# Performance work log

Measured on AMD Instinct MI355X. Metric: run time of the kernel, lower is better.

The kernel has to match this reference:

```python
import jax, jax.numpy as jnp
import numpy as np

D_MODEL = 512
NUM_HEADS = 8
D_K = D_MODEL // NUM_HEADS
SCALE = 1.0 / np.sqrt(D_K).astype(np.float32)


def _relative_shift(x):
    # x: (B, H, S, P) pos scores from Q @ P^T; Transformer-XL shift trick.
    b, h, s, p = x.shape
    x = jnp.pad(x, ((0, 0), (0, 0), (0, 0), (1, 0)))   # (B,H,S,P+1)
    x = x.reshape(b, h, p + 1, s)[:, :, 1:, :]          # drop first row
    x = x.reshape(b, h, s, p)[:, :, :, :s]
    return x


def setup_inputs() -> dict:
    key = jax.random.key(0)
    ks = jax.random.split(key, 10)
    B, S = 4, 2048
    glorot = lambda k: jax.random.uniform(
        k, (D_MODEL, D_MODEL), jnp.float32,
        -np.sqrt(6.0 / (2 * D_MODEL)), np.sqrt(6.0 / (2 * D_MODEL)))
    return {
        "inputs": jax.random.normal(ks[0], (B, S, D_MODEL), jnp.float32),
        "pos_enc": jax.random.normal(ks[1], (1, S, D_MODEL), jnp.float32),
        "W_q": glorot(ks[2]),
        "W_k": glorot(ks[3]),
        "W_v": glorot(ks[4]),
        "W_o": glorot(ks[5]),
        "W_pos": glorot(ks[6]),
        "u_bias": jnp.zeros((NUM_HEADS, D_K), jnp.float32),
        "v_bias": jnp.zeros((NUM_HEADS, D_K), jnp.float32),
    }


def reference(inputs, pos_enc, W_q, W_k, W_v, W_o, W_pos, u_bias, v_bias):
    B, S, _ = inputs.shape
    split = lambda x, b: x.reshape(b, S, NUM_HEADS, D_K).transpose(0, 2, 1, 3)
    Q = split(inputs @ W_q, B)        # (B,H,S,dk)
    K = split(inputs @ W_k, B)
    V = split(inputs @ W_v, B)
    P = split(pos_enc @ W_pos, 1)      # (1,H,S,dk)
    u = u_bias[None, :, None, :]
    v = v_bias[None, :, None, :]
    content_score = jnp.einsum('bhid,bhjd->bhij', Q + u, K)
    pos_score = jnp.einsum('bhid,xhjd->bhij', Q + v, P)  # broadcast over batch
    pos_score = _relative_shift(pos_score)
    scores = (content_score + pos_score) * SCALE
    attn = jax.nn.softmax(scores, axis=-1)  # no dropout (inference)
    context = jnp.einsum('bhij,bhjd->bhid', attn, V)
    context = context.transpose(0, 2, 1, 3).reshape(B, S, D_MODEL)
    return context @ W_o
```

## Files before the change

kernel.cpp:

```cpp
#include <hip/hip_runtime.h>
#include <hip/hip_bf16.h>
#include <math.h>

#define SEQ 2048
#define NH 8
#define DK 64
#define DM 512
#define RSCALE 0.125f
#define PPAD (SEQ + 128)
#define POFF 64
#define KSTR 72
#define PSTR 36

typedef unsigned short ushortT;
typedef short s16x8 __attribute__((ext_vector_type(8)));
typedef float f32x4 __attribute__((ext_vector_type(4)));

#define MFMA16 __builtin_amdgcn_mfma_f32_16x16x32_bf16

static __device__ __forceinline__ ushortT f2bf(float x) {
  __hip_bfloat16 h = __float2bfloat16(x);
  ushortT u;
  __builtin_memcpy(&u, &h, 2);
  return u;
}

static __device__ __forceinline__ f32x4 exp4(f32x4 g) {
  f32x4 r;
  r[0] = __expf(g[0]); r[1] = __expf(g[1]);
  r[2] = __expf(g[2]); r[3] = __expf(g[3]);
  return r;
}

static __device__ __forceinline__ s16x8 pack8(const float* p) {
  ushortT u[8];
#pragma unroll
  for (int i = 0; i < 8; ++i) u[i] = f2bf(p[i]);
  s16x8 out;
  __builtin_memcpy(&out, u, 16);
  return out;
}

static __device__ __forceinline__ int pinv(int j) {
  return (j < 16) ? ((j >> 2) * 8 + (j & 3)) : (((j >> 2) - 4) * 8 + 4 + (j & 3));
}

__global__ __launch_bounds__(256)
void cast_in(const float* __restrict__ X, const float* __restrict__ PE,
             ushortT* __restrict__ Xb, ushortT* __restrict__ PEb) {
  const size_t i4 = (size_t)blockIdx.x * 256 + threadIdx.x;
  const size_t NX = (size_t)4 * SEQ * DM / 4;
  const float4 v = (i4 < NX) ? *(const float4*)(X + i4 * 4)
                             : *(const float4*)(PE + (i4 - NX) * 4);
  ushortT o[4] = {f2bf(v.x), f2bf(v.y), f2bf(v.z), f2bf(v.w)};
  ushortT* dst = (i4 < NX) ? (Xb + i4 * 4) : (PEb + (i4 - NX) * 4);
  *(ulonglong1*)dst = *(ulonglong1*)o;
}

__global__ __launch_bounds__(256)
void transpose_w(const float* __restrict__ w0, const float* __restrict__ w1,
                 const float* __restrict__ w2, const float* __restrict__ w3,
                 const float* __restrict__ w4, ushortT* __restrict__ out) {
  __shared__ float ts[32][33];
  const int z = blockIdx.z;
  const float* w = (z == 0) ? w0 : (z == 1) ? w1 : (z == 2) ? w2 : (z == 3) ? w3 : w4;
  ushortT* o = out + (size_t)z * DM * DM;
  const int k0 = blockIdx.x * 32, n0 = blockIdx.y * 32;
  const int tx = threadIdx.x, ty = threadIdx.y;
#pragma unroll
  for (int i = 0; i < 4; ++i)
    ts[ty + i * 8][tx] = w[(size_t)(k0 + ty + i * 8) * DM + n0 + tx];
  __syncthreads();
#pragma unroll
  for (int i = 0; i < 4; ++i)
    o[(size_t)(n0 + ty + i * 8) * DM + k0 + tx] = f2bf(ts[tx][ty + i * 8]);
}

__global__ __launch_bounds__(256)
void gemm_mfma(const ushortT* __restrict__ A, const ushortT* __restrict__ Bt,
               const float* __restrict__ ubv, const float* __restrict__ vbv,
               ushortT* __restrict__ qu, ushortT* __restrict__ qv,
               ushortT* __restrict__ kb, ushortT* __restrict__ vt,
               float* __restrict__ of, int mode) {
  const int w = threadIdx.x >> 6, lane = threadIdx.x & 63;
  const int c = lane & 15, q = lane >> 4;
  const int m0 = blockIdx.x * 64;
  const int n0 = blockIdx.y * 128 + w * 32;

  const ushortT* Ab = A + (size_t)m0 * DM + q * 8;
  const ushortT* Bb = Bt + (size_t)n0 * DM + q * 8;

  f32x4 acc[4][2];
#pragma unroll
  for (int mt = 0; mt < 4; ++mt)
#pragma unroll
    for (int nt = 0; nt < 2; ++nt) acc[mt][nt] = (f32x4){0.f, 0.f, 0.f, 0.f};

  s16x8 a[4], bfr[2], an[4], bn[2];
#pragma unroll
  for (int mt = 0; mt < 4; ++mt) a[mt] = *(const s16x8*)(Ab + (size_t)(mt * 16 + c) * DM);
#pragma unroll
  for (int nt = 0; nt < 2; ++nt) bfr[nt] = *(const s16x8*)(Bb + (size_t)(nt * 16 + c) * DM);

  for (int k0 = 0; k0 < DM; k0 += 32) {
    if (k0 + 32 < DM) {
#pragma unroll
      for (int mt = 0; mt < 4; ++mt)
        an[mt] = *(const s16x8*)(Ab + (size_t)(mt * 16 + c) * DM + k0 + 32);
#pragma unroll
      for (int nt = 0; nt < 2; ++nt)
        bn[nt] = *(const s16x8*)(Bb + (size_t)(nt * 16 + c) * DM + k0 + 32);
    }
#pragma unroll
    for (int mt = 0; mt < 4; ++mt)
#pragma unroll
      for (int nt = 0; nt < 2; ++nt)
        acc[mt][nt] = MFMA16(a[mt], bfr[nt], acc[mt][nt], 0, 0, 0);
#pragma unroll
    for (int mt = 0; mt < 4; ++mt) a[mt] = an[mt];
#pragma unroll
    for (int nt = 0; nt < 2; ++nt) bfr[nt] = bn[nt];
  }

#pragma unroll
  for (int mt = 0; mt < 4; ++mt)
#pragma unroll
    for (int nt = 0; nt < 2; ++nt)
#pragma unroll
      for (int r = 0; r < 4; ++r) {
        const int gm = m0 + mt * 16 + q * 4 + r;
        const int gn = n0 + nt * 16 + c;
        const float v = acc[mt][nt][r];
        const int bb = gm >> 11, s = gm & (SEQ - 1);
        if (mode == 0) {
          const int z = gn >> 9, gn5 = gn & 511;
          const int h = gn5 >> 6, d = gn5 & 63;
          if (z == 0) {
            const size_t base = (((size_t)bb * NH + h) * SEQ + s) * DK + d;
            qu[base] = f2bf((v + ubv[gn5]) * RSCALE);
            qv[base] = f2bf((v + vbv[gn5]) * RSCALE);
          } else if (z == 1) {
            kb[(((size_t)bb * NH + h) * SEQ + s) * DK + d] = f2bf(v);
          } else {
            const int s_il = (s & ~31) | pinv(s & 31);
            vt[(((size_t)bb * NH + h) * DK + d) * SEQ + s_il] = f2bf(v);
          }
        } else if (mode == 3) {
          const int h = gn >> 6, d = gn & 63;
          qu[((size_t)h * PPAD + POFF + gm) * DK + d] = f2bf(v);
        } else {
          of[(size_t)gm * DM + gn] = v;
        }
      }
}

static __device__ __forceinline__ f32x4 band_gemm(const ushortT* pb, int tile,
                                                  int c, int q, s16x8 a0, s16x8 a1) {
  const ushortT* pc = pb + (ptrdiff_t)(tile * 16 + c) * DK + q * 8;
  f32x4 G = {0.f, 0.f, 0.f, 0.f};
  G = MFMA16(a0, *(const s16x8*)pc, G, 0, 0, 0);
  G = MFMA16(a1, *(const s16x8*)(pc + 32), G, 0, 0, 0);
  return G;
}

__global__ __launch_bounds__(256, 3)
void attn_mfma(const ushortT* __restrict__ Qu, const ushortT* __restrict__ Qv,
               const ushortT* __restrict__ Kb, const ushortT* __restrict__ Vt,
               const ushortT* __restrict__ Pp, ushortT* __restrict__ ctxb) {
  const int n = blockIdx.x;
  const int xcd = n & 7, idx = n >> 3;
  const int b = idx >> 5, iblk = idx & 31;
  const int h = xcd, bh = b * 8 + h;
  const int tid = threadIdx.x;
  const int w = tid >> 6, lane = tid & 63;
  const int c = lane & 15, q = lane >> 4;
  const int i0 = iblk * 64;
  const int iw = i0 + w * 16;

  __shared__ ushortT Ks[64][KSTR];
  __shared__ ushortT Vs[64][KSTR];
  __shared__ float E1[4][16][PSTR];
  __shared__ float E2[4][16][PSTR];
  __shared__ float Lb[4][16];

  const ushortT* Qub = Qu + ((size_t)bh * SEQ + iw) * DK;
  const ushortT* Qvb = Qv + ((size_t)bh * SEQ + iw) * DK;
  const ushortT* Kbh = Kb + (size_t)bh * SEQ * DK;
  const ushortT* Vbh = Vt + (size_t)bh * DK * SEQ;
  const ushortT* Ph  = Pp + ((size_t)h * PPAD + POFF) * DK;

  const s16x8 qu0 = *(const s16x8*)(Qub + (size_t)c * DK + q * 8);
  const s16x8 qu1 = *(const s16x8*)(Qub + (size_t)c * DK + 32 + q * 8);
  s16x8 qv0 = *(const s16x8*)(Qvb + (size_t)c * DK + q * 8);
  s16x8 qv1 = *(const s16x8*)(Qvb + (size_t)c * DK + 32 + q * 8);

  int joff[8];
#pragma unroll
  for (int jj = 0; jj < 8; ++jj)
    joff[jj] = (jj < 4) ? (4 * q + jj) : (16 + 4 * q + (jj - 4));

  f32x4 O[4];
#pragma unroll
  for (int r = 0; r < 4; ++r) O[r] = (f32x4){0.f, 0.f, 0.f, 0.f};
  float lrow = 0.f;
  f32x4 e[3];
  bool hv1 = false, hv2 = false;
  const int jt = iw & ~31;
  const int m_w = q * 4;

  {
    const ushortT* gk = Kbh;
    uint4 k0v = *(const uint4*)(gk + tid * 8);
    uint4 k1v = *(const uint4*)(gk + 2048 + tid * 8);
    const ushortT* gv = Vbh + (size_t)(tid >> 2) * SEQ + (tid & 3) * 16;
    uint4 v0v = *(const uint4*)gv;
    uint4 v1v = *(const uint4*)(gv + 8);
    *(uint4*)&Ks[tid >> 3][(tid & 7) * 8] = k0v;
    *(uint4*)&Ks[32 + (tid >> 3)][(tid & 7) * 8] = k1v;
    *(uint4*)&Vs[tid >> 2][(tid & 3) * 16] = v0v;
    *(uint4*)&Vs[tid >> 2][(tid & 3) * 16 + 8] = v1v;
  }
  __syncthreads();

#define WRITE_BAND(ARR, ev)                                                   \
  _Pragma("unroll")                                                           \
  for (int t = 0; t < 3; ++t)                                                 \
    _Pragma("unroll")                                                         \
    for (int r = 0; r < 4; ++r) {                                             \
      const int kcol = t * 16 + c + (m_w + r) - 15;                           \
      if (kcol >= 0 && kcol < 32) ARR[w][m_w + r][pinv(kcol)] = (ev)[t][r];   \
    }

#define PV_FROM(pr, jl)                                                       \
  {                                                                           \
    lrow += pr[0] + pr[1] + pr[2] + pr[3] + pr[4] + pr[5] + pr[6] + pr[7];    \
    const s16x8 pa = pack8(pr);                                               \
    _Pragma("unroll")                                                         \
    for (int dt = 0; dt < 4; ++dt) {                                          \
      const s16x8 vb = *(const s16x8*)&Vs[dt * 16 + c][(jl) + q * 8];         \
      O[dt] = MFMA16(pa, vb, O[dt], 0, 0, 0);                                 \
    }                                                                         \
  }

  for (int ch = 0; ch < 32; ++ch) {
    const bool more = (ch + 1) < 32;
    uint4 k0v, k1v, v0v, v1v;
    if (more) {
      const ushortT* gk = Kbh + (size_t)(ch + 1) * 64 * DK;
      k0v = *(const uint4*)(gk + tid * 8);
      k1v = *(const uint4*)(gk + 2048 + tid * 8);
      const ushortT* gv = Vbh + (size_t)(tid >> 2) * SEQ + (ch + 1) * 64 + (tid & 3) * 16;
      v0v = *(const uint4*)gv;
      v1v = *(const uint4*)(gv + 8);
    }
#pragma unroll
    for (int t = 0; t < 2; ++t) {
      const int j0 = ch * 64 + t * 32;
      const int jl = t * 32;
      const int drel = j0 - iw;
      f32x4 S0 = {0.f, 0.f, 0.f, 0.f}, S1 = {0.f, 0.f, 0.f, 0.f};
      {
        const ushortT* ka = &Ks[jl + c][q * 8];
        S0 = MFMA16(*(const s16x8*)ka, qu0, S0, 0, 0, 0);
        S0 = MFMA16(*(const s16x8*)(ka + 32), qu1, S0, 0, 0, 0);
        const ushortT* ka2 = &Ks[jl + 16 + c][q * 8];
        S1 = MFMA16(*(const s16x8*)ka2, qu0, S1, 0, 0, 0);
        S1 = MFMA16(*(const s16x8*)(ka2 + 32), qu1, S1, 0, 0, 0);
      }
      if (j0 < jt) {
        const ushortT* pb1 = Ph + (ptrdiff_t)(drel + SEQ - 16) * DK;
        if (hv1) e[0] = e[2];
        else { e[0] = exp4(band_gemm(pb1, 0, c, q, qv0, qv1)); hv1 = true; }
        e[1] = exp4(band_gemm(pb1, 1, c, q, qv0, qv1));
        e[2] = exp4(band_gemm(pb1, 2, c, q, qv0, qv1));
        WRITE_BAND(E1, e)
        const float* e1r = &E1[w][c][q * 8];
        float4 fA = *(const float4*)e1r, fB = *(const float4*)(e1r + 4);
        float pr[8] = {__expf(S0[0]) * fA.x, __expf(S0[1]) * fA.y,
                       __expf(S0[2]) * fA.z, __expf(S0[3]) * fA.w,
                       __expf(S1[0]) * fB.x, __expf(S1[1]) * fB.y,
                       __expf(S1[2]) * fB.z, __expf(S1[3]) * fB.w};
        PV_FROM(pr, jl)
      } else if (j0 < jt + 64) {
        {
          const ushortT* pb1 = Ph + (ptrdiff_t)(drel + SEQ - 16) * DK;
          f32x4 t1[3];
          t1[0] = exp4(band_gemm(pb1, 0, c, q, qv0, qv1));
          t1[1] = exp4(band_gemm(pb1, 1, c, q, qv0, qv1));
          t1[2] = exp4(band_gemm(pb1, 2, c, q, qv0, qv1));
          WRITE_BAND(E1, t1)
        }
        {
          const s16x8 qw0 = *(const s16x8*)(Qvb + (size_t)(c + 1) * DK + q * 8);
          const s16x8 qw1 = *(const s16x8*)(Qvb + (size_t)(c + 1) * DK + 32 + q * 8);
          const ushortT* pb2 = Ph + (ptrdiff_t)(drel - 17) * DK;
          f32x4 t2[3];
          t2[0] = exp4(band_gemm(pb2, 0, c, q, qw0, qw1));
          t2[1] = exp4(band_gemm(pb2, 1, c, q, qw0, qw1));
          t2[2] = exp4(band_gemm(pb2, 2, c, q, qw0, qw1));
          WRITE_BAND(E2, t2)
        }
        const float* e1r = &E1[w][c][q * 8];
        const float* e2r = &E2[w][c][q * 8];
        float4 aA = *(const float4*)e1r, aB = *(const float4*)(e1r + 4);
        float4 bA = *(const float4*)e2r, bB = *(const float4*)(e2r + 4);
        float f1[8] = {aA.x, aA.y, aA.z, aA.w, aB.x, aB.y, aB.z, aB.w};
        float f2[8] = {bA.x, bA.y, bA.z, bA.w, bB.x, bB.y, bB.z, bB.w};
        float es[8] = {__expf(S0[0]), __expf(S0[1]), __expf(S0[2]), __expf(S0[3]),
                       __expf(S1[0]), __expf(S1[1]), __expf(S1[2]), __expf(S1[3])};
        float pr[8];
#pragma unroll
        for (int jj = 0; jj < 8; ++jj) {
          const int dlt = drel + joff[jj] - c;
          const float f = (dlt <= 0) ? f1[jj] : ((dlt == 1) ? 1.0f : f2[jj]);
          pr[jj] = es[jj] * f;
        }
        PV_FROM(pr, jl)
      } else {
        if (!hv2) {
          qv0 = *(const s16x8*)(Qvb + (size_t)(c + 1) * DK + q * 8);
          qv1 = *(const s16x8*)(Qvb + (size_t)(c + 1) * DK + 32 + q * 8);
        }
        const ushortT* pb2 = Ph + (ptrdiff_t)(drel - 17) * DK;
        if (hv2) e[0] = e[2];
        else { e[0] = exp4(band_gemm(pb2, 0, c, q, qv0, qv1)); hv2 = true; }
        e[1] = exp4(band_gemm(pb2, 1, c, q, qv0, qv1));
        e[2] = exp4(band_gemm(pb2, 2, c, q, qv0, qv1));
        WRITE_BAND(E1, e)
        const float* e1r = &E1[w][c][q * 8];
        float4 fA = *(const float4*)e1r, fB = *(const float4*)(e1r + 4);
        float pr[8] = {__expf(S0[0]) * fA.x, __expf(S0[1]) * fA.y,
                       __expf(S0[2]) * fA.z, __expf(S0[3]) * fA.w,
                       __expf(S1[0]) * fB.x, __expf(S1[1]) * fB.y,
                       __expf(S1[2]) * fB.z, __expf(S1[3]) * fB.w};
        PV_FROM(pr, jl)
      }
    }
    __syncthreads();
    if (more) {
      *(uint4*)&Ks[tid >> 3][(tid & 7) * 8] = k0v;
      *(uint4*)&Ks[32 + (tid >> 3)][(tid & 7) * 8] = k1v;
      *(uint4*)&Vs[tid >> 2][(tid & 3) * 16] = v0v;
      *(uint4*)&Vs[tid >> 2][(tid & 3) * 16 + 8] = v1v;
    }
    __syncthreads();
  }

  lrow += __shfl_xor(lrow, 16);
  lrow += __shfl_xor(lrow, 32);
  if (q == 0) Lb[w][c] = lrow;
  float inv[4];
#pragma unroll
  for (int r = 0; r < 4; ++r) inv[r] = 1.0f / Lb[w][q * 4 + r];
#pragma unroll
  for (int dt = 0; dt < 4; ++dt)
#pragma unroll
    for (int r = 0; r < 4; ++r) {
      const int i = iw + q * 4 + r;
      ctxb[((size_t)b * SEQ + i) * DM + h * DK + dt * 16 + c] = f2bf(O[dt][r] * inv[r]);
    }
}

extern "C" void kernel_launch(void* const* d_in, const int* in_sizes, int n_in,
                              void* d_out, int out_size, void* d_ws, size_t ws_size,
                              hipStream_t stream) {
  (void)in_sizes; (void)n_in; (void)out_size; (void)ws_size;
  const float* X   = (const float*)d_in[0];
  const float* PE  = (const float*)d_in[1];
  const float* Wq  = (const float*)d_in[2];
  const float* Wk  = (const float*)d_in[3];
  const float* Wv  = (const float*)d_in[4];
  const float* Wo  = (const float*)d_in[5];
  const float* Wp  = (const float*)d_in[6];
  const float* ubv = (const float*)d_in[7];
  const float* vbv = (const float*)d_in[8];

  const size_t NX = (size_t)4 * SEQ * DM;
  const size_t NP = (size_t)SEQ * DM;
  const size_t NW = (size_t)DM * DM;
  ushortT* Xb  = (ushortT*)d_ws;
  ushortT* PEb = Xb + NX;
  ushortT* Wt  = PEb + NP;
  ushortT* qu  = Wt + 5 * NW;
  ushortT* qv  = qu + NX;
  ushortT* kb  = qv + NX;
  ushortT* vt  = kb + NX;
  ushortT* pp  = vt + NX;
  ushortT* ctx = pp + (size_t)NH * PPAD * DK;
  float* outp = (float*)d_out;

  hipLaunchKernelGGL(cast_in, dim3((NX + NP) / 4 / 256), dim3(256), 0, stream, X, PE, Xb, PEb);
  hipLaunchKernelGGL(transpose_w, dim3(16, 16, 5), dim3(32, 8), 0, stream, Wq, Wk, Wv, Wp, Wo, Wt);
  dim3 blk(256);
  hipLaunchKernelGGL(gemm_mfma, dim3(128, 12), blk, 0, stream, Xb, Wt, ubv, vbv,
                     qu, qv, kb, vt, (float*)nullptr, 0);
  hipLaunchKernelGGL(gemm_mfma, dim3(32, 4), blk, 0, stream, PEb, Wt + 3 * NW, ubv, vbv,
                     pp, (ushortT*)nullptr, (ushortT*)nullptr, (ushortT*)nullptr, (float*)nullptr, 3);
  hipLaunchKernelGGL(attn_mfma, dim3(1024), blk, 0, stream, qu, qv, kb, vt, pp, ctx);
  hipLaunchKernelGGL(gemm_mfma, dim3(128, 4), blk, 0, stream, ctx, Wt + 4 * NW, ubv, vbv,
                     (ushortT*)nullptr, (ushortT*)nullptr, (ushortT*)nullptr, (ushortT*)nullptr, outp, 4);
}
```

Baseline: 408.1 us.

## Double-buffer K in LDS, read V from global, drop E2 buffer for occupancy

V tiles are no longer staged in shared memory; PV MFMA operands are loaded directly from global/L2. K is double-buffered in LDS, which removes one barrier per chunk, and the second band scratch buffer is replaced by reusing E1 sequentially. Launch bounds rise from 3 to 5 blocks per SM to exploit the smaller LDS footprint. The cost is uncoalesced per-lane global V loads and higher register pressure from the tighter launch bound.

```diff
diff --git a/kernel.cpp b/kernel.cpp
--- a/kernel.cpp
+++ b/kernel.cpp
@@ -163,7 +163,7 @@
   return G;
 }
 
-__global__ __launch_bounds__(256, 3)
+__global__ __launch_bounds__(256, 5)
 void attn_mfma(const ushortT* __restrict__ Qu, const ushortT* __restrict__ Qv,
                const ushortT* __restrict__ Kb, const ushortT* __restrict__ Vt,
                const ushortT* __restrict__ Pp, ushortT* __restrict__ ctxb) {
@@ -177,10 +177,8 @@
   const int i0 = iblk * 64;
   const int iw = i0 + w * 16;
 
-  __shared__ ushortT Ks[64][KSTR];
-  __shared__ ushortT Vs[64][KSTR];
+  __shared__ ushortT Ks[2][64][KSTR];
   __shared__ float E1[4][16][PSTR];
-  __shared__ float E2[4][16][PSTR];
   __shared__ float Lb[4][16];
 
   const ushortT* Qub = Qu + ((size_t)bh * SEQ + iw) * DK;
@@ -209,49 +207,41 @@
   const int m_w = q * 4;
 
   {
-    const ushortT* gk = Kbh;
-    uint4 k0v = *(const uint4*)(gk + tid * 8);
-    uint4 k1v = *(const uint4*)(gk + 2048 + tid * 8);
-    const ushortT* gv = Vbh + (size_t)(tid >> 2) * SEQ + (tid & 3) * 16;
-    uint4 v0v = *(const uint4*)gv;
-    uint4 v1v = *(const uint4*)(gv + 8);
-    *(uint4*)&Ks[tid >> 3][(tid & 7) * 8] = k0v;
-    *(uint4*)&Ks[32 + (tid >> 3)][(tid & 7) * 8] = k1v;
-    *(uint4*)&Vs[tid >> 2][(tid & 3) * 16] = v0v;
-    *(uint4*)&Vs[tid >> 2][(tid & 3) * 16 + 8] = v1v;
+    uint4 k0v = *(const uint4*)(Kbh + tid * 8);
+    uint4 k1v = *(const uint4*)(Kbh + 2048 + tid * 8);
+    *(uint4*)&Ks[0][tid >> 3][(tid & 7) * 8] = k0v;
+    *(uint4*)&Ks[0][32 + (tid >> 3)][(tid & 7) * 8] = k1v;
   }
   __syncthreads();
 
-#define WRITE_BAND(ARR, ev)                                                   \
+#define WRITE_BAND(ev)                                                        \
   _Pragma("unroll")                                                           \
   for (int t = 0; t < 3; ++t)                                                 \
     _Pragma("unroll")                                                         \
     for (int r = 0; r < 4; ++r) {                                             \
       const int kcol = t * 16 + c + (m_w + r) - 15;                           \
-      if (kcol >= 0 && kcol < 32) ARR[w][m_w + r][pinv(kcol)] = (ev)[t][r];   \
-    }
-
-#define PV_FROM(pr, jl)                                                       \
+      if (kcol >= 0 && kcol < 32) E1[w][m_w + r][pinv(kcol)] = (ev)[t][r];    \
+    }
+
+#define PV_FROM(pr, j0g)                                                      \
   {                                                                           \
     lrow += pr[0] + pr[1] + pr[2] + pr[3] + pr[4] + pr[5] + pr[6] + pr[7];    \
     const s16x8 pa = pack8(pr);                                               \
     _Pragma("unroll")                                                         \
     for (int dt = 0; dt < 4; ++dt) {                                          \
-      const s16x8 vb = *(const s16x8*)&Vs[dt * 16 + c][(jl) + q * 8];         \
+      const s16x8 vb = *(const s16x8*)(Vbh + (size_t)(dt * 16 + c) * SEQ + (j0g) + q * 8); \
       O[dt] = MFMA16(pa, vb, O[dt], 0, 0, 0);                                 \
     }                                                                         \
   }
 
   for (int ch = 0; ch < 32; ++ch) {
+    const int cur = ch & 1;
     const bool more = (ch + 1) < 32;
-    uint4 k0v, k1v, v0v, v1v;
+    uint4 k0v, k1v;
     if (more) {
       const ushortT* gk = Kbh + (size_t)(ch + 1) * 64 * DK;
       k0v = *(const uint4*)(gk + tid * 8);
       k1v = *(const uint4*)(gk + 2048 + tid * 8);
-      const ushortT* gv = Vbh + (size_t)(tid >> 2) * SEQ + (ch + 1) * 64 + (tid & 3) * 16;
-      v0v = *(const uint4*)gv;
-      v1v = *(const uint4*)(gv + 8);
     }
 #pragma unroll
     for (int t = 0; t < 2; ++t) {
@@ -260,10 +250,10 @@
       const int drel = j0 - iw;
       f32x4 S0 = {0.f, 0.f, 0.f, 0.f}, S1 = {0.f, 0.f, 0.f, 0.f};
       {
-        const ushortT* ka = &Ks[jl + c][q * 8];
+        const ushortT* ka = &Ks[cur][jl + c][q * 8];
         S0 = MFMA16(*(const s16x8*)ka, qu0, S0, 0, 0, 0);
         S0 = MFMA16(*(const s16x8*)(ka + 32), qu1, S0, 0, 0, 0);
-        const ushortT* ka2 = &Ks[jl + 16 + c][q * 8];
+        const ushortT* ka2 = &Ks[cur][jl + 16 + c][q * 8];
         S1 = MFMA16(*(const s16x8*)ka2, qu0, S1, 0, 0, 0);
         S1 = MFMA16(*(const s16x8*)(ka2 + 32), qu1, S1, 0, 0, 0);
       }
@@ -273,22 +263,27 @@
         else { e[0] = exp4(band_gemm(pb1, 0, c, q, qv0, qv1)); hv1 = true; }
         e[1] = exp4(band_gemm(pb1, 1, c, q, qv0, qv1));
         e[2] = exp4(band_gemm(pb1, 2, c, q, qv0, qv1));
-        WRITE_BAND(E1, e)
+        WRITE_BAND(e)
         const float* e1r = &E1[w][c][q * 8];
         float4 fA = *(const float4*)e1r, fB = *(const float4*)(e1r + 4);
         float pr[8] = {__expf(S0[0]) * fA.x, __expf(S0[1]) * fA.y,
                        __expf(S0[2]) * fA.z, __expf(S0[3]) * fA.w,
                        __expf(S1[0]) * fB.x, __expf(S1[1]) * fB.y,
                        __expf(S1[2]) * fB.z, __expf(S1[3]) * fB.w};
-        PV_FROM(pr, jl)
+        PV_FROM(pr, j0)
       } else if (j0 < jt + 64) {
+        float f1[8], f2[8];
         {
           const ushortT* pb1 = Ph + (ptrdiff_t)(drel + SEQ - 16) * DK;
           f32x4 t1[3];
           t1[0] = exp4(band_gemm(pb1, 0, c, q, qv0, qv1));
           t1[1] = exp4(band_gemm(pb1, 1, c, q, qv0, qv1));
           t1[2] = exp4(band_gemm(pb1, 2, c, q, qv0, qv1));
-          WRITE_BAND(E1, t1)
+          WRITE_BAND(t1)
+          const float* e1r = &E1[w][c][q * 8];
+          float4 aA = *(const float4*)e1r, aB = *(const float4*)(e1r + 4);
+          f1[0] = aA.x; f1[1] = aA.y; f1[2] = aA.z; f1[3] = aA.w;
+          f1[4] = aB.x; f1[5] = aB.y; f1[6] = aB.z; f1[7] = aB.w;
         }
         {
           const s16x8 qw0 = *(const s16x8*)(Qvb + (size_t)(c + 1) * DK + q * 8);
@@ -298,14 +293,12 @@
           t2[0] = exp4(band_gemm(pb2, 0, c, q, qw0, qw1));
           t2[1] = exp4(band_gemm(pb2, 1, c, q, qw0, qw1));
           t2[2] = exp4(band_gemm(pb2, 2, c, q, qw0, qw1));
-          WRITE_BAND(E2, t2)
-        }
-        const float* e1r = &E1[w][c][q * 8];
-        const float* e2r = &E2[w][c][q * 8];
-        float4 aA = *(const float4*)e1r, aB = *(const float4*)(e1r + 4);
-        float4 bA = *(const float4*)e2r, bB = *(const float4*)(e2r + 4);
-        float f1[8] = {aA.x, aA.y, aA.z, aA.w, aB.x, aB.y, aB.z, aB.w};
-        float f2[8] = {bA.x, bA.y, bA.z, bA.w, bB.x, bB.y, bB.z, bB.w};
+          WRITE_BAND(t2)
+          const float* e1r = &E1[w][c][q * 8];
+          float4 bA = *(const float4*)e1r, bB = *(const float4*)(e1r + 4);
+          f2[0] = bA.x; f2[1] = bA.y; f2[2] = bA.z; f2[3] = bA.w;
+          f2[4] = bB.x; f2[5] = bB.y; f2[6] = bB.z; f2[7] = bB.w;
+        }
         float es[8] = {__expf(S0[0]), __expf(S0[1]), __expf(S0[2]), __expf(S0[3]),
                        __expf(S1[0]), __expf(S1[1]), __expf(S1[2]), __expf(S1[3])};
         float pr[8];
@@ -315,7 +308,7 @@
           const float f = (dlt <= 0) ? f1[jj] : ((dlt == 1) ? 1.0f : f2[jj]);
           pr[jj] = es[jj] * f;
         }
-        PV_FROM(pr, jl)
+        PV_FROM(pr, j0)
       } else {
         if (!hv2) {
           qv0 = *(const s16x8*)(Qvb + (size_t)(c + 1) * DK + q * 8);
@@ -326,22 +319,19 @@
         else { e[0] = exp4(band_gemm(pb2, 0, c, q, qv0, qv1)); hv2 = true; }
         e[1] = exp4(band_gemm(pb2, 1, c, q, qv0, qv1));
         e[2] = exp4(band_gemm(pb2, 2, c, q, qv0, qv1));
-        WRITE_BAND(E1, e)
+        WRITE_BAND(e)
         const float* e1r = &E1[w][c][q * 8];
         float4 fA = *(const float4*)e1r, fB = *(const float4*)(e1r + 4);
         float pr[8] = {__expf(S0[0]) * fA.x, __expf(S0[1]) * fA.y,
                        __expf(S0[2]) * fA.z, __expf(S0[3]) * fA.w,
                        __expf(S1[0]) * fB.x, __expf(S1[1]) * fB.y,
                        __expf(S1[2]) * fB.z, __expf(S1[3]) * fB.w};
-        PV_FROM(pr, jl)
+        PV_FROM(pr, j0)
       }
     }
-    __syncthreads();
     if (more) {
-      *(uint4*)&Ks[tid >> 3][(tid & 7) * 8] = k0v;
-      *(uint4*)&Ks[32 + (tid >> 3)][(tid & 7) * 8] = k1v;
-      *(uint4*)&Vs[tid >> 2][(tid & 3) * 16] = v0v;
-      *(uint4*)&Vs[tid >> 2][(tid & 3) * 16 + 8] = v1v;
+      *(uint4*)&Ks[1 - cur][tid >> 3][(tid & 7) * 8] = k0v;
+      *(uint4*)&Ks[1 - cur][32 + (tid >> 3)][(tid & 7) * 8] = k1v;
     }
     __syncthreads();
   }
```

After: 640.3 us. +56.9%, slower.

## Stage GEMM operands through LDS with 128x128 block tiles

Applied to the files above, without the earlier changes.

Rewrites the projection GEMM so each 256-thread block loads a 128x128 output tile's A and B k-slices cooperatively into padded shared memory, then each wave reads its MFMA fragments from LDS. Before, each wave loaded its fragments straight from global memory with no sharing across waves. The change is meant to cut redundant global/L2 traffic by reusing operands across the four waves, and it doubles the per-wave tile to 64x64. The cost is two barriers per k-step, fewer blocks in the grid (lower occupancy on the small pos GEMM), and more accumulator registers.

```diff
diff --git a/kernel.cpp b/kernel.cpp
--- a/kernel.cpp
+++ b/kernel.cpp
@@ -11,6 +11,7 @@
 #define POFF 64
 #define KSTR 72
 #define PSTR 36
+#define ASTR 34
 
 typedef unsigned short ushortT;
 typedef short s16x8 __attribute__((ext_vector_type(8)));
@@ -82,54 +83,61 @@
                ushortT* __restrict__ qu, ushortT* __restrict__ qv,
                ushortT* __restrict__ kb, ushortT* __restrict__ vt,
                float* __restrict__ of, int mode) {
-  const int w = threadIdx.x >> 6, lane = threadIdx.x & 63;
+  __shared__ ushortT As[128][ASTR];
+  __shared__ ushortT Bs[128][ASTR];
+  const int tid = threadIdx.x;
+  const int w = tid >> 6, lane = tid & 63;
   const int c = lane & 15, q = lane >> 4;
-  const int m0 = blockIdx.x * 64;
-  const int n0 = blockIdx.y * 128 + w * 32;
-
-  const ushortT* Ab = A + (size_t)m0 * DM + q * 8;
-  const ushortT* Bb = Bt + (size_t)n0 * DM + q * 8;
-
-  f32x4 acc[4][2];
+  const int wm = w >> 1, wn = w & 1;
+  const int m0 = blockIdx.x * 128, n0 = blockIdx.y * 128;
+  const int lr = tid >> 1, lh = (tid & 1) * 16;
+
+  f32x4 acc[4][4];
 #pragma unroll
   for (int mt = 0; mt < 4; ++mt)
 #pragma unroll
-    for (int nt = 0; nt < 2; ++nt) acc[mt][nt] = (f32x4){0.f, 0.f, 0.f, 0.f};
-
-  s16x8 a[4], bfr[2], an[4], bn[2];
-#pragma unroll
-  for (int mt = 0; mt < 4; ++mt) a[mt] = *(const s16x8*)(Ab + (size_t)(mt * 16 + c) * DM);
-#pragma unroll
-  for (int nt = 0; nt < 2; ++nt) bfr[nt] = *(const s16x8*)(Bb + (size_t)(nt * 16 + c) * DM);
+    for (int nt = 0; nt < 4; ++nt) acc[mt][nt] = (f32x4){0.f, 0.f, 0.f, 0.f};
+
+  const ushortT* Ar = A + (size_t)(m0 + lr) * DM + lh;
+  const ushortT* Br = Bt + (size_t)(n0 + lr) * DM + lh;
+  uint4 a0 = *(const uint4*)(Ar);
+  uint4 a1 = *(const uint4*)(Ar + 8);
+  uint4 b0 = *(const uint4*)(Br);
+  uint4 b1 = *(const uint4*)(Br + 8);
 
   for (int k0 = 0; k0 < DM; k0 += 32) {
+    __syncthreads();
+    *(uint4*)&As[lr][lh] = a0; *(uint4*)&As[lr][lh + 8] = a1;
+    *(uint4*)&Bs[lr][lh] = b0; *(uint4*)&Bs[lr][lh + 8] = b1;
+    __syncthreads();
     if (k0 + 32 < DM) {
-#pragma unroll
-      for (int mt = 0; mt < 4; ++mt)
-        an[mt] = *(const s16x8*)(Ab + (size_t)(mt * 16 + c) * DM + k0 + 32);
-#pragma unroll
-      for (int nt = 0; nt < 2; ++nt)
-        bn[nt] = *(const s16x8*)(Bb + (size_t)(nt * 16 + c) * DM + k0 + 32);
-    }
+      a0 = *(const uint4*)(Ar + k0 + 32);
+      a1 = *(const uint4*)(Ar + k0 + 40);
+      b0 = *(const uint4*)(Br + k0 + 32);
+      b1 = *(const uint4*)(Br + k0 + 40);
+    }
+    s16x8 af[4], bf[4];
 #pragma unroll
     for (int mt = 0; mt < 4; ++mt)
-#pragma unroll
-      for (int nt = 0; nt < 2; ++nt)
-        acc[mt][nt] = MFMA16(a[mt], bfr[nt], acc[mt][nt], 0, 0, 0);
-#pragma unroll
-    for (int mt = 0; mt < 4; ++mt) a[mt] = an[mt];
-#pragma unroll
-    for (int nt = 0; nt < 2; ++nt) bfr[nt] = bn[nt];
+      af[mt] = *(const s16x8*)&As[wm * 64 + mt * 16 + c][q * 8];
+#pragma unroll
+    for (int nt = 0; nt < 4; ++nt)
+      bf[nt] = *(const s16x8*)&Bs[wn * 64 + nt * 16 + c][q * 8];
+#pragma unroll
+    for (int mt = 0; mt < 4; ++mt)
+#pragma unroll
+      for (int nt = 0; nt < 4; ++nt)
+        acc[mt][nt] = MFMA16(af[mt], bf[nt], acc[mt][nt], 0, 0, 0);
   }
 
 #pragma unroll
   for (int mt = 0; mt < 4; ++mt)
 #pragma unroll
-    for (int nt = 0; nt < 2; ++nt)
+    for (int nt = 0; nt < 4; ++nt)
 #pragma unroll
       for (int r = 0; r < 4; ++r) {
-        const int gm = m0 + mt * 16 + q * 4 + r;
-        const int gn = n0 + nt * 16 + c;
+        const int gm = m0 + wm * 64 + mt * 16 + q * 4 + r;
+        const int gn = n0 + wn * 64 + nt * 16 + c;
         const float v = acc[mt][nt][r];
         const int bb = gm >> 11, s = gm & (SEQ - 1);
         if (mode == 0) {
@@ -392,11 +400,11 @@
   hipLaunchKernelGGL(cast_in, dim3((NX + NP) / 4 / 256), dim3(256), 0, stream, X, PE, Xb, PEb);
   hipLaunchKernelGGL(transpose_w, dim3(16, 16, 5), dim3(32, 8), 0, stream, Wq, Wk, Wv, Wp, Wo, Wt);
   dim3 blk(256);
-  hipLaunchKernelGGL(gemm_mfma, dim3(128, 12), blk, 0, stream, Xb, Wt, ubv, vbv,
+  hipLaunchKernelGGL(gemm_mfma, dim3(64, 12), blk, 0, stream, Xb, Wt, ubv, vbv,
                      qu, qv, kb, vt, (float*)nullptr, 0);
-  hipLaunchKernelGGL(gemm_mfma, dim3(32, 4), blk, 0, stream, PEb, Wt + 3 * NW, ubv, vbv,
+  hipLaunchKernelGGL(gemm_mfma, dim3(16, 4), blk, 0, stream, PEb, Wt + 3 * NW, ubv, vbv,
                      pp, (ushortT*)nullptr, (ushortT*)nullptr, (ushortT*)nullptr, (float*)nullptr, 3);
   hipLaunchKernelGGL(attn_mfma, dim3(1024), blk, 0, stream, qu, qv, kb, vt, pp, ctx);
-  hipLaunchKernelGGL(gemm_mfma, dim3(128, 4), blk, 0, stream, ctx, Wt + 4 * NW, ubv, vbv,
+  hipLaunchKernelGGL(gemm_mfma, dim3(64, 4), blk, 0, stream, ctx, Wt + 4 * NW, ubv, vbv,
                      (ushortT*)nullptr, (ushortT*)nullptr, (ushortT*)nullptr, (ushortT*)nullptr, outp, 4);
 }
```

After: 370.4 us. 9.2% less time.
